# Kernel tuning notes

Measured on AMD Instinct MI355X. Metric: run time of the kernel, lower is better.

## Reference

```python
import jax, jax.numpy as jnp
import numpy as np

N, E, D, L, POS_VOC = 50000, 800000, 128, 3, 1024
EPS = 1e-5  # torch LayerNorm default


def layer_norm(x, g, b):
    m = jnp.mean(x, axis=-1, keepdims=True)
    v = jnp.var(x, axis=-1, keepdims=True)
    return (x - m) * jax.lax.rsqrt(v + EPS) * g + b


def setup_inputs() -> dict:
    key = jax.random.key(0)
    ks = jax.random.split(key, 8)
    node_emb = jax.random.normal(ks[0], (N, D), jnp.float32)
    pos = jax.random.randint(ks[1], (N,), 0, POS_VOC, dtype=jnp.int32)
    edge = jax.random.randint(ks[2], (2, E), 0, N, dtype=jnp.int32)
    # pos_embedding: xavier-uniform rows 1:, padding_idx=0 row zeroed
    lim = np.sqrt(6.0 / (POS_VOC - 1 + D))
    pos_table = jax.random.uniform(ks[3], (POS_VOC, D), jnp.float32, -lim, lim)
    pos_table = pos_table.at[0].set(0.0)
    # SAGEConv per layer: lin_l (with bias) on aggregated neighbors, lin_r (no bias) on root
    Wl = jax.random.normal(ks[4], (L, D, D), jnp.float32) / np.sqrt(D)
    bl = jnp.zeros((L, D), jnp.float32)
    Wr = jax.random.normal(ks[5], (L, D, D), jnp.float32) / np.sqrt(D)
    emb_ln_g = jnp.ones((D,), jnp.float32)
    emb_ln_b = jnp.zeros((D,), jnp.float32)
    hid_ln_g = jnp.ones((L, D), jnp.float32)
    hid_ln_b = jnp.zeros((L, D), jnp.float32)
    return dict(node_emb=node_emb, pos=pos, edge=edge, pos_table=pos_table,
                Wl=Wl, bl=bl, Wr=Wr, emb_ln_g=emb_ln_g, emb_ln_b=emb_ln_b,
                hid_ln_g=hid_ln_g, hid_ln_b=hid_ln_b)


def reference(node_emb, pos, edge, pos_table, Wl, bl, Wr,
              emb_ln_g, emb_ln_b, hid_ln_g, hid_ln_b):
    # embedding: scaled node emb + position embedding, then LayerNorm (dropout p=0 -> identity)
    x = node_emb * np.float32(np.sqrt(D)) + pos_table[pos]        # [N, D]
    x = layer_norm(x, emb_ln_g, emb_ln_b)
    src, dst = edge[0], edge[1]
    for i in range(L):
        # SAGEConv(aggr='add'): scatter-add neighbor feats, transform, add root transform
        agg = jax.ops.segment_sum(x[src], dst, num_segments=N)    # [N, D]
        h = agg @ Wl[i] + bl[i] + x @ Wr[i]                       # [N, D]
        h = jax.nn.relu(h)
        x = layer_norm(h + x, hid_ln_g[i], hid_ln_b[i])           # residual + LN
    return x
```

## Files before the change

### kernel.cpp

```cpp
#include <hip/hip_runtime.h>

#define DDIM    128
#define NNODES  50000
#define NEDGES  800000
#define NLAYERS 3
#define LN_EPS  1e-5f
#define CAP     96
#define NSLICE  8
#define SLICESZ ((NNODES + NSLICE - 1) / NSLICE)
#define FILL_EPT 8
#define FILL_CHUNK (256 * FILL_EPT)
#define FILL_NCHUNK ((NEDGES + FILL_CHUNK - 1) / FILL_CHUNK)

#define FILLB  (FILL_NCHUNK * NSLICE)
#define WPACKB ((NLAYERS * 4096 + 255) / 256)
#define EMBEDB ((NNODES + 15) / 16)

typedef short s16x8 __attribute__((ext_vector_type(8)));
typedef float f32x4 __attribute__((ext_vector_type(4)));
typedef unsigned int u32;

__device__ __forceinline__ unsigned short f2bf(float f) {
    union { float f; unsigned u; } c; c.f = f;
    unsigned r = c.u + 0x7fff + ((c.u >> 16) & 1);
    return (unsigned short)(r >> 16);
}
__device__ __forceinline__ float bf2f_u(unsigned short h) {
    union { unsigned u; float f; } c; c.u = (unsigned)h << 16;
    return c.f;
}
__device__ __forceinline__ float bflo(u32 v) { return __uint_as_float(v << 16); }
__device__ __forceinline__ float bfhi(u32 v) { return __uint_as_float(v & 0xffff0000u); }

__global__ __launch_bounds__(256) void prep_kernel(
    const int* __restrict__ edge,
    int* __restrict__ cursor, int* __restrict__ srcs,
    const float* __restrict__ Wl, const float* __restrict__ Wr,
    unsigned short* __restrict__ wpk,
    const float* __restrict__ node_emb, const int* __restrict__ pos,
    const float* __restrict__ pos_table,
    const float* __restrict__ eg, const float* __restrict__ eb,
    uint4* __restrict__ xh4)
{
    int t = threadIdx.x;

    if (blockIdx.x < FILLB) {
        int slice = blockIdx.x & (NSLICE - 1);
        int chunk = blockIdx.x >> 3;
        int lo = slice * SLICESZ;
        int hi = lo + SLICESZ;
        int base = chunk * FILL_CHUNK + t;
        #pragma unroll
        for (int i = 0; i < FILL_EPT; ++i) {
            int e = base + i * 256;
            if (e < NEDGES) {
                int d = edge[NEDGES + e];
                if (d >= lo && d < hi) {
                    int s = edge[e];
                    int slot = atomicAdd(&cursor[d], 1);
                    srcs[d * CAP + slot] = s;
                }
            }
        }
        return;
    }

    if (blockIdx.x < FILLB + WPACKB) {
        int idx = (blockIdx.x - FILLB) * 256 + t;
        if (idx >= NLAYERS * 4096) return;
        int l   = idx >> 12;
        int rem = idx & 4095;
        int kt = rem >> 9, ct = (rem >> 6) & 7, ln = rem & 63;
        int k0 = kt * 32 + ((ln >> 4) << 3);
        int c  = ct * 16 + (ln & 15);
        const float* src = (kt < 4)
            ? Wl + (size_t)l * DDIM * DDIM + (size_t)k0 * DDIM + c
            : Wr + (size_t)l * DDIM * DDIM + (size_t)(k0 - 128) * DDIM + c;
        s16x8 o;
        #pragma unroll
        for (int j = 0; j < 8; ++j) o[j] = (short)f2bf(src[j * DDIM]);
        *(s16x8*)(wpk + (size_t)idx * 8) = o;
        return;
    }

    int bi = blockIdx.x - FILLB - WPACKB;
    int wv = (bi * 256 + t) >> 6;
    int lane = t & 63;
    int h = lane >> 4;
    int L = lane & 15;
    int n = wv * 4 + h;
    if (n >= NNODES) return;

    const float scale = 11.313708498984761f;
    int p = pos[n];

    const float* nb = node_emb + (size_t)n * DDIM + L * 8;
    const float* pb = pos_table + (size_t)p * DDIM + L * 8;
    float4 ne0 = *(const float4*)(nb);
    float4 ne1 = *(const float4*)(nb + 4);
    float4 pt0 = *(const float4*)(pb);
    float4 pt1 = *(const float4*)(pb + 4);

    float v[8];
    v[0] = ne0.x * scale + pt0.x;  v[1] = ne0.y * scale + pt0.y;
    v[2] = ne0.z * scale + pt0.z;  v[3] = ne0.w * scale + pt0.w;
    v[4] = ne1.x * scale + pt1.x;  v[5] = ne1.y * scale + pt1.y;
    v[6] = ne1.z * scale + pt1.z;  v[7] = ne1.w * scale + pt1.w;

    float s = 0.f, s2 = 0.f;
    #pragma unroll
    for (int k = 0; k < 8; ++k) { s += v[k]; s2 += v[k] * v[k]; }
    #pragma unroll
    for (int m = 8; m > 0; m >>= 1) {
        s  += __shfl_xor(s,  m, 64);
        s2 += __shfl_xor(s2, m, 64);
    }
    float mean = s * (1.0f / DDIM);
    float var  = s2 * (1.0f / DDIM) - mean * mean;
    float rstd = rsqrtf(var + LN_EPS);

    float4 gv0 = *(const float4*)(eg + L * 8);
    float4 gv1 = *(const float4*)(eg + L * 8 + 4);
    float4 bv0 = *(const float4*)(eb + L * 8);
    float4 bv1 = *(const float4*)(eb + L * 8 + 4);
    float gq[8] = {gv0.x, gv0.y, gv0.z, gv0.w, gv1.x, gv1.y, gv1.z, gv1.w};
    float bq[8] = {bv0.x, bv0.y, bv0.z, bv0.w, bv1.x, bv1.y, bv1.z, bv1.w};

    float y[8];
    #pragma unroll
    for (int k = 0; k < 8; ++k) y[k] = (v[k] - mean) * rstd * gq[k] + bq[k];

    uint4 o;
    o.x = (u32)f2bf(y[0]) | ((u32)f2bf(y[1]) << 16);
    o.y = (u32)f2bf(y[2]) | ((u32)f2bf(y[3]) << 16);
    o.z = (u32)f2bf(y[4]) | ((u32)f2bf(y[5]) << 16);
    o.w = (u32)f2bf(y[6]) | ((u32)f2bf(y[7]) << 16);
    xh4[(size_t)n * 16 + L] = o;
}

__global__ __launch_bounds__(256) void gather_kernel(
    const int* __restrict__ deg,
    const int* __restrict__ srcs,
    const uint4* __restrict__ xh4,
    uint4* __restrict__ agg4)
{
    int wid  = (blockIdx.x * 256 + threadIdx.x) >> 6;
    int lane = threadIdx.x & 63;
    if (wid >= NNODES) return;
    int q = lane >> 4, cl = lane & 15;

    int beg = wid * CAP;
    int end = beg + deg[wid];

    float acc[8];
    #pragma unroll
    for (int k = 0; k < 8; ++k) acc[k] = 0.0f;

    for (int j = beg; j < end; j += 32) {
        int sidx[8];
        #pragma unroll
        for (int c = 0; c < 8; ++c) {
            int jj = j + c * 4 + q;
            sidx[c] = (jj < end) ? srcs[jj] : -1;
        }
        uint4 u[8];
        #pragma unroll
        for (int c = 0; c < 8; ++c) {
            u[c] = make_uint4(0u, 0u, 0u, 0u);
            if (sidx[c] >= 0)
                u[c] = xh4[(size_t)sidx[c] * 16 + cl];
        }
        #pragma unroll
        for (int c = 0; c < 8; ++c) {
            acc[0] += bflo(u[c].x); acc[1] += bfhi(u[c].x);
            acc[2] += bflo(u[c].y); acc[3] += bfhi(u[c].y);
            acc[4] += bflo(u[c].z); acc[5] += bfhi(u[c].z);
            acc[6] += bflo(u[c].w); acc[7] += bfhi(u[c].w);
        }
    }

    #pragma unroll
    for (int k = 0; k < 8; ++k) {
        acc[k] += __shfl_xor(acc[k], 16, 64);
        acc[k] += __shfl_xor(acc[k], 32, 64);
    }

    if (q == 0) {
        uint4 o;
        o.x = (u32)f2bf(acc[0]) | ((u32)f2bf(acc[1]) << 16);
        o.y = (u32)f2bf(acc[2]) | ((u32)f2bf(acc[3]) << 16);
        o.z = (u32)f2bf(acc[4]) | ((u32)f2bf(acc[5]) << 16);
        o.w = (u32)f2bf(acc[6]) | ((u32)f2bf(acc[7]) << 16);
        agg4[(size_t)wid * 16 + cl] = o;
    }
}

__global__ __launch_bounds__(256) void sage_mfma_kernel(
    const unsigned short* __restrict__ agg,
    unsigned short* __restrict__ xh,
    const unsigned short* __restrict__ wpk,
    const float* __restrict__ bl,
    const float* __restrict__ g,
    const float* __restrict__ b,
    float* __restrict__ xout)
{
    __shared__ unsigned short wlds[4096 * 8];

    int t    = threadIdx.x;
    int wave = t >> 6;
    int lane = t & 63;
    int cl   = lane & 15;
    int q    = lane >> 4;

    {
        const s16x8* srcv = (const s16x8*)wpk;
        s16x8* dstv = (s16x8*)wlds;
        for (int i = t; i < 4096; i += 256) dstv[i] = srcv[i];
    }
    __syncthreads();

    float bias[8], gg[8], bb[8];
    #pragma unroll
    for (int ct = 0; ct < 8; ++ct) {
        int c = ct * 16 + cl;
        bias[ct] = bl[c]; gg[ct] = g[c]; bb[ct] = b[c];
    }

    int m0 = blockIdx.x * 64 + wave * 16;
    int m  = m0 + cl;
    int mc = (m < NNODES) ? m : (NNODES - 1);

    s16x8 af[8];
    #pragma unroll
    for (int kt = 0; kt < 4; ++kt)
        af[kt] = *(const s16x8*)(agg + (size_t)mc * DDIM + kt * 32 + q * 8);
    #pragma unroll
    for (int kt = 4; kt < 8; ++kt)
        af[kt] = *(const s16x8*)(xh + (size_t)mc * DDIM + (kt - 4) * 32 + q * 8);

    f32x4 acc[8];
    #pragma unroll
    for (int ct = 0; ct < 8; ++ct) acc[ct] = (f32x4){0.f, 0.f, 0.f, 0.f};

    #pragma unroll
    for (int kt = 0; kt < 8; ++kt) {
        #pragma unroll
        for (int ct = 0; ct < 8; ++ct) {
            s16x8 bfr = *(const s16x8*)&wlds[((((kt << 3) + ct) << 6) + lane) * 8];
            acc[ct] = __builtin_amdgcn_mfma_f32_16x16x32_bf16(af[kt], bfr, acc[ct], 0, 0, 0);
        }
    }

    float hbuf[8][4];
    #pragma unroll
    for (int ct = 0; ct < 8; ++ct) {
        #pragma unroll
        for (int r = 0; r < 4; ++r) {
            int node = m0 + q * 4 + r;
            int nc   = (node < NNODES) ? node : (NNODES - 1);
            float hv = fmaxf(acc[ct][r] + bias[ct], 0.0f);
            hbuf[ct][r] = hv + bf2f_u(xh[(size_t)nc * DDIM + ct * 16 + cl]);
        }
    }

    float s[4], s2[4];
    #pragma unroll
    for (int r = 0; r < 4; ++r) {
        float a0 = 0.f, a1 = 0.f;
        #pragma unroll
        for (int ct = 0; ct < 8; ++ct) {
            a0 += hbuf[ct][r];
            a1 += hbuf[ct][r] * hbuf[ct][r];
        }
        #pragma unroll
        for (int msk = 1; msk < 16; msk <<= 1) {
            a0 += __shfl_xor(a0, msk, 64);
            a1 += __shfl_xor(a1, msk, 64);
        }
        s[r] = a0; s2[r] = a1;
    }

    #pragma unroll
    for (int r = 0; r < 4; ++r) {
        int node = m0 + q * 4 + r;
        if (node >= NNODES) continue;
        float mean = s[r] * (1.0f / DDIM);
        float var  = s2[r] * (1.0f / DDIM) - mean * mean;
        float rstd = rsqrtf(var + LN_EPS);
        #pragma unroll
        for (int ct = 0; ct < 8; ++ct) {
            float y = (hbuf[ct][r] - mean) * rstd * gg[ct] + bb[ct];
            size_t off = (size_t)node * DDIM + ct * 16 + cl;
            if (xout) xout[off] = y;
            else      xh[off]   = f2bf(y);
        }
    }
}

extern "C" void kernel_launch(void* const* d_in, const int* in_sizes, int n_in,
                              void* d_out, int out_size, void* d_ws, size_t ws_size,
                              hipStream_t stream)
{
    const float* node_emb = (const float*)d_in[0];
    const int*   pos      = (const int*)d_in[1];
    const int*   edge     = (const int*)d_in[2];
    const float* pos_tab  = (const float*)d_in[3];
    const float* Wl       = (const float*)d_in[4];
    const float* bl       = (const float*)d_in[5];
    const float* Wr       = (const float*)d_in[6];
    const float* eg       = (const float*)d_in[7];
    const float* eb       = (const float*)d_in[8];
    const float* hg       = (const float*)d_in[9];
    const float* hb       = (const float*)d_in[10];

    unsigned short* xh  = (unsigned short*)d_ws;
    unsigned short* agg = xh + (size_t)NNODES * DDIM;
    unsigned short* wpk = agg + (size_t)NNODES * DDIM;
    int* cursor = (int*)(wpk + (size_t)NLAYERS * 4096 * 8);
    int* srcs   = cursor + NNODES;

    hipMemsetAsync(cursor, 0, NNODES * sizeof(int), stream);
    prep_kernel<<<FILLB + WPACKB + EMBEDB, 256, 0, stream>>>(
        edge, cursor, srcs, Wl, Wr, wpk,
        node_emb, pos, pos_tab, eg, eb, (uint4*)xh);

    for (int l = 0; l < NLAYERS; ++l) {
        gather_kernel<<<(NNODES * 64 + 255) / 256, 256, 0, stream>>>(
            cursor, srcs, (const uint4*)xh, (uint4*)agg);

        sage_mfma_kernel<<<(NNODES + 63) / 64, 256, 0, stream>>>(
            agg, xh,
            wpk + (size_t)l * 4096 * 8,
            bl + (size_t)l * DDIM,
            hg + (size_t)l * DDIM,
            hb + (size_t)l * DDIM,
            (l == NLAYERS - 1) ? (float*)d_out : (float*)nullptr);
    }
}
```

Before: 279.6 us.

## Fuse neighbor gather into SAGE MFMA kernel with LDS aggregation and ping-pong buffers

Merges the per-layer gather kernel into the MFMA transform kernel. Each block first aggregates its 64 nodes' neighbors into a swizzled LDS tile, then feeds that tile directly to the MFMA without a global round trip. Node features are ping-ponged between two buffers so that reads during gather do not race with writes from other blocks. The edge fill also switches to vectorized int4 loads with contiguous edges per thread. The trade-offs are fewer gather lanes per node (16 lanes per node, 4 nodes per wave), which may reduce memory-level parallelism, and more LDS per block.

```diff
diff --git a/kernel.cpp b/kernel.cpp
--- a/kernel.cpp
+++ b/kernel.cpp
@@ -49,16 +49,20 @@
         int chunk = blockIdx.x >> 3;
         int lo = slice * SLICESZ;
         int hi = lo + SLICESZ;
-        int base = chunk * FILL_CHUNK + t;
-        #pragma unroll
-        for (int i = 0; i < FILL_EPT; ++i) {
-            int e = base + i * 256;
-            if (e < NEDGES) {
-                int d = edge[NEDGES + e];
+        int base = chunk * FILL_CHUNK + t * FILL_EPT;
+        if (base < NEDGES) {
+            int4 d0 = *(const int4*)(edge + NEDGES + base);
+            int4 d1 = *(const int4*)(edge + NEDGES + base + 4);
+            int4 s0 = *(const int4*)(edge + base);
+            int4 s1 = *(const int4*)(edge + base + 4);
+            int dd[8] = {d0.x, d0.y, d0.z, d0.w, d1.x, d1.y, d1.z, d1.w};
+            int ss[8] = {s0.x, s0.y, s0.z, s0.w, s1.x, s1.y, s1.z, s1.w};
+            #pragma unroll
+            for (int i = 0; i < 8; ++i) {
+                int d = dd[i];
                 if (d >= lo && d < hi) {
-                    int s = edge[e];
                     int slot = atomicAdd(&cursor[d], 1);
-                    srcs[d * CAP + slot] = s;
+                    srcs[d * CAP + slot] = ss[i];
                 }
             }
         }
@@ -138,84 +142,73 @@
     xh4[(size_t)n * 16 + L] = o;
 }
 
-__global__ __launch_bounds__(256) void gather_kernel(
+__global__ __launch_bounds__(256) void sage_fused_kernel(
     const int* __restrict__ deg,
     const int* __restrict__ srcs,
-    const uint4* __restrict__ xh4,
-    uint4* __restrict__ agg4)
+    const uint4* __restrict__ xin4,
+    const unsigned short* __restrict__ xin,
+    const unsigned short* __restrict__ wpk,
+    const float* __restrict__ bl,
+    const float* __restrict__ g,
+    const float* __restrict__ b,
+    unsigned short* __restrict__ xh_out,
+    float* __restrict__ xout)
 {
-    int wid  = (blockIdx.x * 256 + threadIdx.x) >> 6;
-    int lane = threadIdx.x & 63;
-    if (wid >= NNODES) return;
-    int q = lane >> 4, cl = lane & 15;
-
-    int beg = wid * CAP;
-    int end = beg + deg[wid];
-
-    float acc[8];
-    #pragma unroll
-    for (int k = 0; k < 8; ++k) acc[k] = 0.0f;
-
-    for (int j = beg; j < end; j += 32) {
-        int sidx[8];
-        #pragma unroll
-        for (int c = 0; c < 8; ++c) {
-            int jj = j + c * 4 + q;
-            sidx[c] = (jj < end) ? srcs[jj] : -1;
-        }
-        uint4 u[8];
-        #pragma unroll
-        for (int c = 0; c < 8; ++c) {
-            u[c] = make_uint4(0u, 0u, 0u, 0u);
-            if (sidx[c] >= 0)
-                u[c] = xh4[(size_t)sidx[c] * 16 + cl];
-        }
-        #pragma unroll
-        for (int c = 0; c < 8; ++c) {
-            acc[0] += bflo(u[c].x); acc[1] += bfhi(u[c].x);
-            acc[2] += bflo(u[c].y); acc[3] += bfhi(u[c].y);
-            acc[4] += bflo(u[c].z); acc[5] += bfhi(u[c].z);
-            acc[6] += bflo(u[c].w); acc[7] += bfhi(u[c].w);
-        }
-    }
-
-    #pragma unroll
-    for (int k = 0; k < 8; ++k) {
-        acc[k] += __shfl_xor(acc[k], 16, 64);
-        acc[k] += __shfl_xor(acc[k], 32, 64);
-    }
-
-    if (q == 0) {
+    __shared__ unsigned short wlds[4096 * 8];
+    __shared__ uint4 aggl[64 * 16];
+
+    int t    = threadIdx.x;
+    int wave = t >> 6;
+    int lane = t & 63;
+    int cl   = lane & 15;
+    int q    = lane >> 4;
+
+    {
+        const s16x8* srcv = (const s16x8*)wpk;
+        s16x8* dstv = (s16x8*)wlds;
+        #pragma unroll
+        for (int i = 0; i < 16; ++i) dstv[t + i * 256] = srcv[t + i * 256];
+    }
+
+    int m0 = blockIdx.x * 64;
+
+    for (int r = 0; r < 4; ++r) {
+        int nl = wave * 16 + r * 4 + q;
+        int n  = m0 + nl;
+        float acc[8];
+        #pragma unroll
+        for (int k = 0; k < 8; ++k) acc[k] = 0.f;
+        if (n < NNODES) {
+            int dg  = deg[n];
+            int beg = n * CAP;
+            for (int j = 0; j < dg; j += 8) {
+                int sidx[8];
+                #pragma unroll
+                for (int c = 0; c < 8; ++c) {
+                    int jj = j + c;
+                    sidx[c] = (jj < dg) ? srcs[beg + jj] : -1;
+                }
+                uint4 u[8];
+                #pragma unroll
+                for (int c = 0; c < 8; ++c) {
+                    u[c] = make_uint4(0u, 0u, 0u, 0u);
+                    if (sidx[c] >= 0) u[c] = xin4[(size_t)sidx[c] * 16 + cl];
+                }
+                #pragma unroll
+                for (int c = 0; c < 8; ++c) {
+                    acc[0] += bflo(u[c].x); acc[1] += bfhi(u[c].x);
+                    acc[2] += bflo(u[c].y); acc[3] += bfhi(u[c].y);
+                    acc[4] += bflo(u[c].z); acc[5] += bfhi(u[c].z);
+                    acc[6] += bflo(u[c].w); acc[7] += bfhi(u[c].w);
+                }
+            }
+        }
         uint4 o;
         o.x = (u32)f2bf(acc[0]) | ((u32)f2bf(acc[1]) << 16);
         o.y = (u32)f2bf(acc[2]) | ((u32)f2bf(acc[3]) << 16);
         o.z = (u32)f2bf(acc[4]) | ((u32)f2bf(acc[5]) << 16);
         o.w = (u32)f2bf(acc[6]) | ((u32)f2bf(acc[7]) << 16);
-        agg4[(size_t)wid * 16 + cl] = o;
-    }
-}
-
-__global__ __launch_bounds__(256) void sage_mfma_kernel(
-    const unsigned short* __restrict__ agg,
-    unsigned short* __restrict__ xh,
-    const unsigned short* __restrict__ wpk,
-    const float* __restrict__ bl,
-    const float* __restrict__ g,
-    const float* __restrict__ b,
-    float* __restrict__ xout)
-{
-    __shared__ unsigned short wlds[4096 * 8];
-
-    int t    = threadIdx.x;
-    int wave = t >> 6;
-    int lane = t & 63;
-    int cl   = lane & 15;
-    int q    = lane >> 4;
-
-    {
-        const s16x8* srcv = (const s16x8*)wpk;
-        s16x8* dstv = (s16x8*)wlds;
-        for (int i = t; i < 4096; i += 256) dstv[i] = srcv[i];
+        aggl[nl * 16 + (cl ^ (nl & 7))] = o;
     }
     __syncthreads();
 
@@ -226,28 +219,29 @@
         bias[ct] = bl[c]; gg[ct] = g[c]; bb[ct] = b[c];
     }
 
-    int m0 = blockIdx.x * 64 + wave * 16;
-    int m  = m0 + cl;
+    int wbase = m0 + wave * 16;
+    int mrow  = wave * 16 + cl;
+    int m  = wbase + cl;
     int mc = (m < NNODES) ? m : (NNODES - 1);
 
     s16x8 af[8];
     #pragma unroll
     for (int kt = 0; kt < 4; ++kt)
-        af[kt] = *(const s16x8*)(agg + (size_t)mc * DDIM + kt * 32 + q * 8);
+        af[kt] = *(const s16x8*)&aggl[mrow * 16 + ((kt * 4 + q) ^ (cl & 7))];
     #pragma unroll
     for (int kt = 4; kt < 8; ++kt)
-        af[kt] = *(const s16x8*)(xh + (size_t)mc * DDIM + (kt - 4) * 32 + q * 8);
-
-    f32x4 acc[8];
-    #pragma unroll
-    for (int ct = 0; ct < 8; ++ct) acc[ct] = (f32x4){0.f, 0.f, 0.f, 0.f};
+        af[kt] = *(const s16x8*)(xin + (size_t)mc * DDIM + (kt - 4) * 32 + q * 8);
+
+    f32x4 accm[8];
+    #pragma unroll
+    for (int ct = 0; ct < 8; ++ct) accm[ct] = (f32x4){0.f, 0.f, 0.f, 0.f};
 
     #pragma unroll
     for (int kt = 0; kt < 8; ++kt) {
         #pragma unroll
         for (int ct = 0; ct < 8; ++ct) {
             s16x8 bfr = *(const s16x8*)&wlds[((((kt << 3) + ct) << 6) + lane) * 8];
-            acc[ct] = __builtin_amdgcn_mfma_f32_16x16x32_bf16(af[kt], bfr, acc[ct], 0, 0, 0);
+            accm[ct] = __builtin_amdgcn_mfma_f32_16x16x32_bf16(af[kt], bfr, accm[ct], 0, 0, 0);
         }
     }
 
@@ -255,44 +249,44 @@
     #pragma unroll
     for (int ct = 0; ct < 8; ++ct) {
         #pragma unroll
-        for (int r = 0; r < 4; ++r) {
-            int node = m0 + q * 4 + r;
+        for (int rr = 0; rr < 4; ++rr) {
+            int node = wbase + q * 4 + rr;
             int nc   = (node < NNODES) ? node : (NNODES - 1);
-            float hv = fmaxf(acc[ct][r] + bias[ct], 0.0f);
-            hbuf[ct][r] = hv + bf2f_u(xh[(size_t)nc * DDIM + ct * 16 + cl]);
+            float hv = fmaxf(accm[ct][rr] + bias[ct], 0.0f);
+            hbuf[ct][rr] = hv + bf2f_u(xin[(size_t)nc * DDIM + ct * 16 + cl]);
         }
     }
 
     float s[4], s2[4];
     #pragma unroll
-    for (int r = 0; r < 4; ++r) {
+    for (int rr = 0; rr < 4; ++rr) {
         float a0 = 0.f, a1 = 0.f;
         #pragma unroll
         for (int ct = 0; ct < 8; ++ct) {
-            a0 += hbuf[ct][r];
-            a1 += hbuf[ct][r] * hbuf[ct][r];
+            a0 += hbuf[ct][rr];
+            a1 += hbuf[ct][rr] * hbuf[ct][rr];
         }
         #pragma unroll
         for (int msk = 1; msk < 16; msk <<= 1) {
             a0 += __shfl_xor(a0, msk, 64);
             a1 += __shfl_xor(a1, msk, 64);
         }
-        s[r] = a0; s2[r] = a1;
-    }
-
-    #pragma unroll
-    for (int r = 0; r < 4; ++r) {
-        int node = m0 + q * 4 + r;
+        s[rr] = a0; s2[rr] = a1;
+    }
+
+    #pragma unroll
+    for (int rr = 0; rr < 4; ++rr) {
+        int node = wbase + q * 4 + rr;
         if (node >= NNODES) continue;
-        float mean = s[r] * (1.0f / DDIM);
-        float var  = s2[r] * (1.0f / DDIM) - mean * mean;
+        float mean = s[rr] * (1.0f / DDIM);
+        float var  = s2[rr] * (1.0f / DDIM) - mean * mean;
         float rstd = rsqrtf(var + LN_EPS);
         #pragma unroll
         for (int ct = 0; ct < 8; ++ct) {
-            float y = (hbuf[ct][r] - mean) * rstd * gg[ct] + bb[ct];
+            float y = (hbuf[ct][rr] - mean) * rstd * gg[ct] + bb[ct];
             size_t off = (size_t)node * DDIM + ct * 16 + cl;
-            if (xout) xout[off] = y;
-            else      xh[off]   = f2bf(y);
+            if (xout) xout[off]    = y;
+            else      xh_out[off]  = f2bf(y);
         }
     }
 }
@@ -313,27 +307,26 @@
     const float* hg       = (const float*)d_in[9];
     const float* hb       = (const float*)d_in[10];
 
-    unsigned short* xh  = (unsigned short*)d_ws;
-    unsigned short* agg = xh + (size_t)NNODES * DDIM;
-    unsigned short* wpk = agg + (size_t)NNODES * DDIM;
+    unsigned short* xA  = (unsigned short*)d_ws;
+    unsigned short* xB  = xA + (size_t)NNODES * DDIM;
+    unsigned short* wpk = xB + (size_t)NNODES * DDIM;
     int* cursor = (int*)(wpk + (size_t)NLAYERS * 4096 * 8);
     int* srcs   = cursor + NNODES;
 
     hipMemsetAsync(cursor, 0, NNODES * sizeof(int), stream);
     prep_kernel<<<FILLB + WPACKB + EMBEDB, 256, 0, stream>>>(
         edge, cursor, srcs, Wl, Wr, wpk,
-        node_emb, pos, pos_tab, eg, eb, (uint4*)xh);
+        node_emb, pos, pos_tab, eg, eb, (uint4*)xA);
 
     for (int l = 0; l < NLAYERS; ++l) {
-        gather_kernel<<<(NNODES * 64 + 255) / 256, 256, 0, stream>>>(
-            cursor, srcs, (const uint4*)xh, (uint4*)agg);
-
-        sage_mfma_kernel<<<(NNODES + 63) / 64, 256, 0, stream>>>(
-            agg, xh,
+        unsigned short* xin = (l & 1) ? xB : xA;
+        unsigned short* xo  = (l & 1) ? xA : xB;
+        sage_fused_kernel<<<(NNODES + 63) / 64, 256, 0, stream>>>(
+            cursor, srcs, (const uint4*)xin, xin,
             wpk + (size_t)l * 4096 * 8,
             bl + (size_t)l * DDIM,
             hg + (size_t)l * DDIM,
             hb + (size_t)l * DDIM,
-            (l == NLAYERS - 1) ? (float*)d_out : (float*)nullptr);
-    }
-}
+            xo, (l == NLAYERS - 1) ? (float*)d_out : (float*)nullptr);
+    }
+}
```

Result: no change. 280.7 us (+0.4%).
